# Optimization experiments

Measured on AMD Instinct MI355X. Metric: run time of the kernel, lower is better.

## Reference

```python
import jax, jax.numpy as jnp
import numpy as np

NU = 100000  # num 'user' nodes
NI = 100000  # num 'item' nodes
E = 600000   # edges per relation
IN_DIM = 128
HID = 128
OUT = 64


def setup_inputs() -> dict:
    key = jax.random.key(0)
    ks = jax.random.split(key, 14)
    return {
        "x_user": jax.random.normal(ks[0], (NU, IN_DIM), jnp.float32),
        "x_item": jax.random.normal(ks[1], (NI, IN_DIM), jnp.float32),
        "W_proj": jax.random.normal(ks[2], (IN_DIM, HID), jnp.float32) / np.sqrt(IN_DIM),
        "b_proj": jax.random.normal(ks[3], (HID,), jnp.float32) * 0.01,
        "W_out": jax.random.normal(ks[4], (HID, OUT), jnp.float32) / np.sqrt(HID),
        "b_out": jax.random.normal(ks[5], (OUT,), jnp.float32) * 0.01,
        "al1": jax.random.normal(ks[6], (1,), jnp.float32),
        "ar1": jax.random.normal(ks[7], (1,), jnp.float32),
        "al2": jax.random.normal(ks[8], (1,), jnp.float32),
        "ar2": jax.random.normal(ks[9], (1,), jnp.float32),
        "e1_src": jax.random.randint(ks[10], (E,), 0, NU, jnp.int32),  # user->user
        "e1_dst": jax.random.randint(ks[11], (E,), 0, NU, jnp.int32),
        "e2_src": jax.random.randint(ks[12], (E,), 0, NI, jnp.int32),  # item->user
        "e2_dst": jax.random.randint(ks[13], (E,), 0, NU, jnp.int32),
    }


def reference(x_user, x_item, W_proj, b_proj, W_out, b_out,
              al1, ar1, al2, ar2, e1_src, e1_dst, e2_src, e2_dst):
    # Shared projection for every node type
    h_user = x_user @ W_proj + b_proj  # [NU, HID]
    h_item = x_item @ W_proj + b_proj  # [NI, HID]

    # Relation ('user','u2u','user'): msg = h_src*al + h_dst*ar, scatter-add to dst
    msg1 = h_user[e1_src] * al1 + h_user[e1_dst] * ar1  # [E, HID]
    out_user = jax.ops.segment_sum(msg1, e1_dst, num_segments=NU)

    # Relation ('item','i2u','user')
    msg2 = h_item[e2_src] * al2 + h_user[e2_dst] * ar2  # [E, HID]
    out_user = out_user + jax.ops.segment_sum(msg2, e2_dst, num_segments=NU)

    # 'item' receives no messages -> zeros
    out_item = jnp.zeros_like(h_item)

    out_user = jax.nn.elu(out_user)
    out_item = jax.nn.elu(out_item)

    # out_layer applied only to 'user'
    out_user = out_user @ W_out + b_out  # [NU, OUT]
    return out_user, out_item
```

## Files before the change

kernel.cpp:

```cpp
#include <hip/hip_runtime.h>
#include <hip/hip_bf16.h>
#include <math.h>

#define NUSER 100000
#define NITEM 100000
#define NEDGE 600000
#define HID   128
#define OUTD  64
#define LDA   136
#define LDF   132
#define BLKR  32
#define PROJ_BLOCKS ((NUSER + NITEM) / BLKR)
#define EPB   ((2 * NEDGE) / PROJ_BLOCKS)

typedef __attribute__((ext_vector_type(8))) short  bf16x8;
typedef __attribute__((ext_vector_type(4))) float  f32x4;
typedef __attribute__((ext_vector_type(4))) unsigned short u16x4;

__device__ inline unsigned short f2bf(float f) {
    __hip_bfloat16 h = __float2bfloat16(f);
    return *reinterpret_cast<unsigned short*>(&h);
}

__device__ inline void bf2x(unsigned int u, float& lo, float& hi) {
    union { unsigned int i; float f; } a, b;
    a.i = u << 16;
    b.i = u & 0xffff0000u;
    lo = a.f; hi = b.f;
}

__global__ void prep(const float* __restrict__ W, unsigned short* __restrict__ wt,
                     int* __restrict__ deg) {
    int i = blockIdx.x * 256 + threadIdx.x;
    if (i < 2 * NUSER) deg[i] = 0;
    if (i < 128 * 128) {
        int k = i >> 7, c = i & 127;
        wt[c * 128 + k] = f2bf(W[i]);
    }
}

__device__ inline void cr_one(int i, const int* e1d, const int* e2d,
                              int* deg1, int* deg2, int* rank) {
    if (i < NEDGE)            rank[i] = atomicAdd(&deg1[e1d[i]], 1);
    else if (i < 2 * NEDGE)   rank[i] = atomicAdd(&deg2[e2d[i - NEDGE]], 1);
}

__global__ void count_rank(const int* __restrict__ e1d, const int* __restrict__ e2d,
                           int* __restrict__ deg1, int* __restrict__ deg2,
                           int* __restrict__ rank) {
    int i0 = blockIdx.x * 512 + threadIdx.x;
    cr_one(i0, e1d, e2d, deg1, deg2, rank);
    cr_one(i0 + 256, e1d, e2d, deg1, deg2, rank);
}

#define SCAN_BLOCKS 391

__global__ __launch_bounds__(256) void scanA(
    const int* __restrict__ deg1, const int* __restrict__ deg2,
    int* __restrict__ off, int* __restrict__ bsum)
{
    __shared__ int sh[256];
    int t = threadIdx.x;
    int i = blockIdx.x * 256 + t;
    int d = (i < NUSER) ? deg1[i] + deg2[i] : 0;
    sh[t] = d;
    __syncthreads();
    for (int dd = 1; dd < 256; dd <<= 1) {
        int v = (t >= dd) ? sh[t - dd] : 0;
        __syncthreads();
        sh[t] += v;
        __syncthreads();
    }
    if (i < NUSER) off[i] = (t > 0) ? sh[t - 1] : 0;
    if (t == 255) bsum[blockIdx.x] = sh[255];
}

__global__ __launch_bounds__(512) void scanB(int* __restrict__ bsum, int* __restrict__ off) {
    __shared__ int sh[512];
    int t = threadIdx.x;
    int v = (t < SCAN_BLOCKS) ? bsum[t] : 0;
    sh[t] = v;
    __syncthreads();
    for (int dd = 1; dd < 512; dd <<= 1) {
        int x = (t >= dd) ? sh[t - dd] : 0;
        __syncthreads();
        sh[t] += x;
        __syncthreads();
    }
    if (t < SCAN_BLOCKS) bsum[t] = (t > 0) ? sh[t - 1] : 0;
    if (t == 511) off[NUSER] = sh[511];
}

__global__ __launch_bounds__(256) void scanC(int* __restrict__ off, const int* __restrict__ bsum) {
    int i = blockIdx.x * 256 + threadIdx.x;
    if (i < NUSER) off[i] += bsum[blockIdx.x];
}

__global__ __launch_bounds__(256) void proj_fill(
    const float* __restrict__ xu, const float* __restrict__ xi,
    const unsigned short* __restrict__ wt, const float* __restrict__ b,
    unsigned short* __restrict__ h,
    const int* __restrict__ e1s, const int* __restrict__ e1d,
    const int* __restrict__ e2s, const int* __restrict__ e2d,
    const int* __restrict__ off, const int* __restrict__ deg1,
    const int* __restrict__ rank, int* __restrict__ adj)
{
    __shared__ unsigned short Al[BLKR * LDA];
    const int tid = threadIdx.x;
    const int r0  = blockIdx.x * BLKR;

    int fsrc = 0, fdst = -1, frank = 0, frel2 = 0;
    if (tid < EPB) {
        int i = blockIdx.x * EPB + tid;
        if (i < NEDGE) {
            fsrc = e1s[i];  fdst = e1d[i];  frank = rank[i];
        } else {
            int j = i - NEDGE;
            fsrc = NUSER + e2s[j];  fdst = e2d[j];  frank = rank[i];  frel2 = 1;
        }
    }

    float4 v[4];
    #pragma unroll
    for (int j = 0; j < 4; j++) {
        int i = tid + j * 256;
        int row = i >> 5, c4 = i & 31;
        int gr = r0 + row;
        const float* srcp = (gr < NUSER) ? xu + (size_t)gr * 128
                                         : xi + (size_t)(gr - NUSER) * 128;
        v[j] = ((const float4*)srcp)[c4];
    }
    __builtin_amdgcn_sched_barrier(0);
    #pragma unroll
    for (int j = 0; j < 4; j++) {
        int i = tid + j * 256;
        int row = i >> 5, c4 = i & 31;
        u16x4 p;
        p.x = f2bf(v[j].x); p.y = f2bf(v[j].y); p.z = f2bf(v[j].z); p.w = f2bf(v[j].w);
        *(u16x4*)&Al[row * LDA + c4 * 4] = p;
    }

    int foff = 0, fd1 = 0;
    if (fdst >= 0) {
        foff = off[fdst];
        if (frel2) fd1 = deg1[fdst];
    }
    __syncthreads();

    const int w    = tid >> 6;
    const int lane = tid & 63;
    const int lrow = lane & 15;
    const int lk   = (lane >> 4) * 8;

    bf16x8 bfrag[4][2];
    #pragma unroll
    for (int kc = 0; kc < 4; kc++) {
        const int ko = kc * 32 + lk;
        bfrag[kc][0] = *(const bf16x8*)&wt[(size_t)(w * 32 + lrow) * 128 + ko];
        bfrag[kc][1] = *(const bf16x8*)&wt[(size_t)(w * 32 + 16 + lrow) * 128 + ko];
    }

    f32x4 acc[2][2] = {};
    #pragma unroll
    for (int kc = 0; kc < 4; kc++) {
        const int ko = kc * 32 + lk;
        #pragma unroll
        for (int rt = 0; rt < 2; rt++) {
            bf16x8 aa = *(const bf16x8*)&Al[(rt * 16 + lrow) * LDA + ko];
            acc[rt][0] = __builtin_amdgcn_mfma_f32_16x16x32_bf16(aa, bfrag[kc][0], acc[rt][0], 0, 0, 0);
            acc[rt][1] = __builtin_amdgcn_mfma_f32_16x16x32_bf16(aa, bfrag[kc][1], acc[rt][1], 0, 0, 0);
        }
    }

    __syncthreads();
    const float bv0 = b[w * 32 + lrow];
    const float bv1 = b[w * 32 + 16 + lrow];
    #pragma unroll
    for (int rt = 0; rt < 2; rt++) {
        #pragma unroll
        for (int ct = 0; ct < 2; ct++) {
            int col = w * 32 + ct * 16 + lrow;
            float bv = ct ? bv1 : bv0;
            #pragma unroll
            for (int r = 0; r < 4; r++) {
                int row = rt * 16 + (lane >> 4) * 4 + r;
                Al[row * LDA + col] = f2bf(acc[rt][ct][r] + bv);
            }
        }
    }
    __syncthreads();

    #pragma unroll
    for (int j = 0; j < 2; j++) {
        int i = tid + j * 256;
        int row = i >> 4, c8 = i & 15;
        *(bf16x8*)&h[(size_t)(r0 + row) * 128 + c8 * 8] =
            *(const bf16x8*)&Al[row * LDA + c8 * 8];
    }

    if (fdst >= 0)
        adj[foff + fd1 + frank] = fsrc;
}

__global__ __launch_bounds__(256) void gather(
    const unsigned short* __restrict__ h, const int* __restrict__ adj,
    const int* __restrict__ off, const int* __restrict__ deg1,
    const int* __restrict__ deg2,
    const float* __restrict__ al1p, const float* __restrict__ ar1p,
    const float* __restrict__ al2p, const float* __restrict__ ar2p,
    unsigned int* __restrict__ accb, float* __restrict__ oitem)
{
    {
        size_t zi = (size_t)blockIdx.x * 256 + threadIdx.x;
        ((float4*)oitem)[zi] = make_float4(0.f, 0.f, 0.f, 0.f);
    }

    int wv   = (int)((blockIdx.x * 256 + threadIdx.x) >> 6);
    int lane = threadIdx.x & 63;
    if (wv >= NUSER / 2) return;
    const int nA = 2 * wv, nB = 2 * wv + 1;

    const unsigned int* h32 = (const unsigned int*)h;
    const float al1 = al1p[0], al2 = al2p[0];
    const float ar1 = ar1p[0], ar2 = ar2p[0];

    int offA = off[nA], offM = off[nA + 1], offE = off[nA + 2];
    const float scA = ar1 * (float)deg1[nA] + ar2 * (float)deg2[nA];
    const float scB = ar1 * (float)deg1[nB] + ar2 * (float)deg2[nB];

    float xA, yA, xB, yB;
    bf2x(h32[(size_t)nA * 64 + lane], xA, yA);
    bf2x(h32[(size_t)nB * 64 + lane], xB, yB);
    float sxA = scA * xA, syA = scA * yA;
    float sxB = scB * xB, syB = scB * yB;

    int eA = offA, endA = offM;
    int eB = offM, endB = offE;

    while (eA + 4 <= endA && eB + 4 <= endB) {
        int sA[4], sB[4];
        #pragma unroll
        for (int j = 0; j < 4; j++) { sA[j] = adj[eA + j]; sB[j] = adj[eB + j]; }
        unsigned int uA[4], uB[4];
        #pragma unroll
        for (int j = 0; j < 4; j++) {
            uA[j] = h32[(size_t)sA[j] * 64 + lane];
            uB[j] = h32[(size_t)sB[j] * 64 + lane];
        }
        #pragma unroll
        for (int j = 0; j < 4; j++) {
            float a = (sA[j] < NUSER) ? al1 : al2;
            float x, y; bf2x(uA[j], x, y);
            sxA = fmaf(a, x, sxA); syA = fmaf(a, y, syA);
            float b2 = (sB[j] < NUSER) ? al1 : al2;
            bf2x(uB[j], x, y);
            sxB = fmaf(b2, x, sxB); syB = fmaf(b2, y, syB);
        }
        eA += 4; eB += 4;
    }
    while (eA + 4 <= endA) {
        int s[4];
        #pragma unroll
        for (int j = 0; j < 4; j++) s[j] = adj[eA + j];
        unsigned int u[4];
        #pragma unroll
        for (int j = 0; j < 4; j++) u[j] = h32[(size_t)s[j] * 64 + lane];
        #pragma unroll
        for (int j = 0; j < 4; j++) {
            float a = (s[j] < NUSER) ? al1 : al2;
            float x, y; bf2x(u[j], x, y);
            sxA = fmaf(a, x, sxA); syA = fmaf(a, y, syA);
        }
        eA += 4;
    }
    for (; eA < endA; eA++) {
        int s0 = adj[eA];
        float a = (s0 < NUSER) ? al1 : al2;
        float x, y; bf2x(h32[(size_t)s0 * 64 + lane], x, y);
        sxA = fmaf(a, x, sxA); syA = fmaf(a, y, syA);
    }
    while (eB + 4 <= endB) {
        int s[4];
        #pragma unroll
        for (int j = 0; j < 4; j++) s[j] = adj[eB + j];
        unsigned int u[4];
        #pragma unroll
        for (int j = 0; j < 4; j++) u[j] = h32[(size_t)s[j] * 64 + lane];
        #pragma unroll
        for (int j = 0; j < 4; j++) {
            float a = (s[j] < NUSER) ? al1 : al2;
            float x, y; bf2x(u[j], x, y);
            sxB = fmaf(a, x, sxB); syB = fmaf(a, y, syB);
        }
        eB += 4;
    }
    for (; eB < endB; eB++) {
        int s0 = adj[eB];
        float a = (s0 < NUSER) ? al1 : al2;
        float x, y; bf2x(h32[(size_t)s0 * 64 + lane], x, y);
        sxB = fmaf(a, x, sxB); syB = fmaf(a, y, syB);
    }

    sxA = sxA > 0.f ? sxA : expm1f(sxA);
    syA = syA > 0.f ? syA : expm1f(syA);
    sxB = sxB > 0.f ? sxB : expm1f(sxB);
    syB = syB > 0.f ? syB : expm1f(syB);
    accb[(size_t)nA * 64 + lane] = ((unsigned int)f2bf(syA) << 16) | (unsigned int)f2bf(sxA);
    accb[(size_t)nB * 64 + lane] = ((unsigned int)f2bf(syB) << 16) | (unsigned int)f2bf(sxB);
}

__global__ __launch_bounds__(256) void finalize(
    const unsigned int* __restrict__ accb, const float* __restrict__ Wo,
    const float* __restrict__ bo, float* __restrict__ out)
{
    __shared__ float Wl[128 * 64];
    __shared__ float Al[64 * LDF];
    const int tid = threadIdx.x;
    const int n0  = blockIdx.x * 64;

    for (int i = tid; i < 128 * 64 / 4; i += 256)
        ((float4*)Wl)[i] = ((const float4*)Wo)[i];

    for (int i = tid; i < 4096; i += 256) {
        int row = i >> 6, d = i & 63;
        int gr = n0 + row;
        float lo = 0.f, hi = 0.f;
        if (gr < NUSER) bf2x(accb[(size_t)gr * 64 + d], lo, hi);
        *(float2*)&Al[row * LDF + d * 2] = make_float2(lo, hi);
    }
    __syncthreads();

    const int tr = tid >> 4;
    const int tc = tid & 15;

    float s[4][4];
    {
        float4 bv = *(const float4*)&bo[tc * 4];
        #pragma unroll
        for (int i = 0; i < 4; i++) {
            s[i][0] = bv.x; s[i][1] = bv.y; s[i][2] = bv.z; s[i][3] = bv.w;
        }
    }

    for (int k0 = 0; k0 < 128; k0 += 4) {
        float4 av[4];
        #pragma unroll
        for (int i = 0; i < 4; i++)
            av[i] = *(const float4*)&Al[(tr * 4 + i) * LDF + k0];
        #pragma unroll
        for (int kk = 0; kk < 4; kk++) {
            float4 wv = *(const float4*)&Wl[(k0 + kk) * 64 + tc * 4];
            #pragma unroll
            for (int i = 0; i < 4; i++) {
                float a = (&av[i].x)[kk];
                s[i][0] = fmaf(a, wv.x, s[i][0]);
                s[i][1] = fmaf(a, wv.y, s[i][1]);
                s[i][2] = fmaf(a, wv.z, s[i][2]);
                s[i][3] = fmaf(a, wv.w, s[i][3]);
            }
        }
    }

    #pragma unroll
    for (int i = 0; i < 4; i++) {
        int gr = n0 + tr * 4 + i;
        if (gr < NUSER) {
            float4 o = make_float4(s[i][0], s[i][1], s[i][2], s[i][3]);
            *(float4*)&out[(size_t)gr * 64 + tc * 4] = o;
        }
    }
}

extern "C" void kernel_launch(void* const* d_in, const int* in_sizes, int n_in,
                              void* d_out, int out_size, void* d_ws, size_t ws_size,
                              hipStream_t stream) {
    const float* xu  = (const float*)d_in[0];
    const float* xi  = (const float*)d_in[1];
    const float* Wp  = (const float*)d_in[2];
    const float* bp  = (const float*)d_in[3];
    const float* Wo  = (const float*)d_in[4];
    const float* bo  = (const float*)d_in[5];
    const float* al1 = (const float*)d_in[6];
    const float* ar1 = (const float*)d_in[7];
    const float* al2 = (const float*)d_in[8];
    const float* ar2 = (const float*)d_in[9];
    const int* e1s = (const int*)d_in[10];
    const int* e1d = (const int*)d_in[11];
    const int* e2s = (const int*)d_in[12];
    const int* e2d = (const int*)d_in[13];

    float* out   = (float*)d_out;
    float* oitem = out + (size_t)NUSER * OUTD;

    unsigned short* h    = (unsigned short*)d_ws;
    unsigned short* wt   = h + (size_t)(NUSER + NITEM) * HID;
    unsigned int*   accb = (unsigned int*)(wt + 128 * 128);

    int* meta = (int*)out;
    int* deg1 = meta;
    int* deg2 = meta + NUSER;
    int* off  = meta + 2 * NUSER;
    int* bsum = meta + 3 * NUSER + 64;
    int* adj  = meta + 3 * NUSER + 1024;
    int* rank = adj + 2 * NEDGE;

    prep<<<(2 * NUSER + 255) / 256, 256, 0, stream>>>(Wp, wt, deg1);

    count_rank<<<(2 * NEDGE + 511) / 512, 256, 0, stream>>>(e1d, e2d, deg1, deg2, rank);

    scanA<<<SCAN_BLOCKS, 256, 0, stream>>>(deg1, deg2, off, bsum);
    scanB<<<1, 512, 0, stream>>>(bsum, off);
    scanC<<<SCAN_BLOCKS, 256, 0, stream>>>(off, bsum);

    proj_fill<<<PROJ_BLOCKS, 256, 0, stream>>>(xu, xi, wt, bp, h,
                                               e1s, e1d, e2s, e2d,
                                               off, deg1, rank, adj);

    gather<<<(NUSER / 2 * 64) / 256, 256, 0, stream>>>(h, adj, off, deg1, deg2,
                                                       al1, ar1, al2, ar2, accb, oitem);

    finalize<<<(NUSER + 63) / 64, 256, 0, stream>>>(accb, Wo, bo, out);
}
```

Before: 229.6 us.

## Build CSR adjacency via two-level bucket binning instead of per-edge global rank atomics

```diff
diff --git a/kernel.cpp b/kernel.cpp
--- a/kernel.cpp
+++ b/kernel.cpp
@@ -11,7 +11,7 @@
 #define LDF   132
 #define BLKR  32
 #define PROJ_BLOCKS ((NUSER + NITEM) / BLKR)
-#define EPB   ((2 * NEDGE) / PROJ_BLOCKS)
+#define NB    ((NUSER + 127) / 128)
 
 typedef __attribute__((ext_vector_type(8))) short  bf16x8;
 typedef __attribute__((ext_vector_type(4))) float  f32x4;
@@ -30,27 +30,27 @@
 }
 
 __global__ void prep(const float* __restrict__ W, unsigned short* __restrict__ wt,
-                     int* __restrict__ deg) {
+                     int* __restrict__ deg, int* __restrict__ bcur) {
     int i = blockIdx.x * 256 + threadIdx.x;
     if (i < 2 * NUSER) deg[i] = 0;
+    if (i < NB) bcur[i] = 0;
     if (i < 128 * 128) {
         int k = i >> 7, c = i & 127;
         wt[c * 128 + k] = f2bf(W[i]);
     }
 }
 
-__device__ inline void cr_one(int i, const int* e1d, const int* e2d,
-                              int* deg1, int* deg2, int* rank) {
-    if (i < NEDGE)            rank[i] = atomicAdd(&deg1[e1d[i]], 1);
-    else if (i < 2 * NEDGE)   rank[i] = atomicAdd(&deg2[e2d[i - NEDGE]], 1);
-}
-
-__global__ void count_rank(const int* __restrict__ e1d, const int* __restrict__ e2d,
-                           int* __restrict__ deg1, int* __restrict__ deg2,
-                           int* __restrict__ rank) {
+__device__ inline void cd_one(int i, const int* e1d, const int* e2d,
+                              int* deg1, int* deg2) {
+    if (i < NEDGE)            atomicAdd(&deg1[e1d[i]], 1);
+    else if (i < 2 * NEDGE)   atomicAdd(&deg2[e2d[i - NEDGE]], 1);
+}
+
+__global__ void count_deg(const int* __restrict__ e1d, const int* __restrict__ e2d,
+                          int* __restrict__ deg1, int* __restrict__ deg2) {
     int i0 = blockIdx.x * 512 + threadIdx.x;
-    cr_one(i0, e1d, e2d, deg1, deg2, rank);
-    cr_one(i0 + 256, e1d, e2d, deg1, deg2, rank);
+    cd_one(i0, e1d, e2d, deg1, deg2);
+    cd_one(i0 + 256, e1d, e2d, deg1, deg2);
 }
 
 #define SCAN_BLOCKS 391
@@ -96,29 +96,61 @@
     if (i < NUSER) off[i] += bsum[blockIdx.x];
 }
 
-__global__ __launch_bounds__(256) void proj_fill(
+__global__ void bin_edges(const int* __restrict__ e1s, const int* __restrict__ e1d,
+                          const int* __restrict__ e2s, const int* __restrict__ e2d,
+                          const int* __restrict__ off, int* __restrict__ bcur,
+                          int2* __restrict__ pairs) {
+    int i = blockIdx.x * 256 + threadIdx.x;
+    if (i >= 2 * NEDGE) return;
+    int src, dst;
+    if (i < NEDGE) { src = e1s[i];                 dst = e1d[i]; }
+    else           { int j = i - NEDGE; src = NUSER + e2s[j]; dst = e2d[j]; }
+    int bkt = dst >> 7;
+    int pos = atomicAdd(&bcur[bkt], 1);
+    pairs[off[bkt << 7] + pos] = make_int2(src, dst);
+}
+
+__global__ __launch_bounds__(256) void place(
+    const int2* __restrict__ pairs, const int* __restrict__ off,
+    const int* __restrict__ deg1, int* __restrict__ adj)
+{
+    __shared__ int offL[129];
+    __shared__ int d1L[128];
+    __shared__ int cnt[256];
+    const int b  = blockIdx.x;
+    const int t  = threadIdx.x;
+    const int d0 = b << 7;
+
+    if (t < 129) {
+        int gi = d0 + t;
+        offL[t] = (gi <= NUSER) ? off[gi] : off[NUSER];
+    }
+    if (t < 128) {
+        int gi = d0 + t;
+        d1L[t] = (gi < NUSER) ? deg1[gi] : 0;
+    }
+    cnt[t] = 0;
+    __syncthreads();
+
+    const int base = offL[0];
+    const int end  = offL[128];
+    for (int e = base + t; e < end; e += 256) {
+        int2 p = pairs[e];
+        int src = p.x, dl = p.y - d0;
+        int rel = (src >= NUSER) ? 1 : 0;
+        int r = atomicAdd(&cnt[dl * 2 + rel], 1);
+        adj[offL[dl] + (rel ? d1L[dl] : 0) + r] = src;
+    }
+}
+
+__global__ __launch_bounds__(256) void proj(
     const float* __restrict__ xu, const float* __restrict__ xi,
     const unsigned short* __restrict__ wt, const float* __restrict__ b,
-    unsigned short* __restrict__ h,
-    const int* __restrict__ e1s, const int* __restrict__ e1d,
-    const int* __restrict__ e2s, const int* __restrict__ e2d,
-    const int* __restrict__ off, const int* __restrict__ deg1,
-    const int* __restrict__ rank, int* __restrict__ adj)
+    unsigned short* __restrict__ h)
 {
     __shared__ unsigned short Al[BLKR * LDA];
     const int tid = threadIdx.x;
     const int r0  = blockIdx.x * BLKR;
-
-    int fsrc = 0, fdst = -1, frank = 0, frel2 = 0;
-    if (tid < EPB) {
-        int i = blockIdx.x * EPB + tid;
-        if (i < NEDGE) {
-            fsrc = e1s[i];  fdst = e1d[i];  frank = rank[i];
-        } else {
-            int j = i - NEDGE;
-            fsrc = NUSER + e2s[j];  fdst = e2d[j];  frank = rank[i];  frel2 = 1;
-        }
-    }
 
     float4 v[4];
     #pragma unroll
@@ -138,12 +170,6 @@
         u16x4 p;
         p.x = f2bf(v[j].x); p.y = f2bf(v[j].y); p.z = f2bf(v[j].z); p.w = f2bf(v[j].w);
         *(u16x4*)&Al[row * LDA + c4 * 4] = p;
-    }
-
-    int foff = 0, fd1 = 0;
-    if (fdst >= 0) {
-        foff = off[fdst];
-        if (frel2) fd1 = deg1[fdst];
     }
     __syncthreads();
 
@@ -197,9 +223,6 @@
         *(bf16x8*)&h[(size_t)(r0 + row) * 128 + c8 * 8] =
             *(const bf16x8*)&Al[row * LDA + c8 * 8];
     }
-
-    if (fdst >= 0)
-        adj[foff + fd1 + frank] = fsrc;
 }
 
 __global__ __launch_bounds__(256) void gather(
@@ -396,25 +419,29 @@
     unsigned short* wt   = h + (size_t)(NUSER + NITEM) * HID;
     unsigned int*   accb = (unsigned int*)(wt + 128 * 128);
 
-    int* meta = (int*)out;
-    int* deg1 = meta;
-    int* deg2 = meta + NUSER;
-    int* off  = meta + 2 * NUSER;
-    int* bsum = meta + 3 * NUSER + 64;
-    int* adj  = meta + 3 * NUSER + 1024;
-    int* rank = adj + 2 * NEDGE;
-
-    prep<<<(2 * NUSER + 255) / 256, 256, 0, stream>>>(Wp, wt, deg1);
-
-    count_rank<<<(2 * NEDGE + 511) / 512, 256, 0, stream>>>(e1d, e2d, deg1, deg2, rank);
+    int* meta  = (int*)out;
+    int* deg1  = meta;
+    int* deg2  = meta + NUSER;
+    int* off   = meta + 2 * NUSER;
+    int* bsum  = meta + 3 * NUSER + 64;
+    int* adj   = meta + 3 * NUSER + 1024;
+    int2* pairs = (int2*)(adj + 2 * NEDGE);
+    int* bcur  = adj + 2 * NEDGE + 4 * NEDGE;
+
+    prep<<<(2 * NUSER + 255) / 256, 256, 0, stream>>>(Wp, wt, deg1, bcur);
+
+    count_deg<<<(2 * NEDGE + 511) / 512, 256, 0, stream>>>(e1d, e2d, deg1, deg2);
 
     scanA<<<SCAN_BLOCKS, 256, 0, stream>>>(deg1, deg2, off, bsum);
     scanB<<<1, 512, 0, stream>>>(bsum, off);
     scanC<<<SCAN_BLOCKS, 256, 0, stream>>>(off, bsum);
 
-    proj_fill<<<PROJ_BLOCKS, 256, 0, stream>>>(xu, xi, wt, bp, h,
-                                               e1s, e1d, e2s, e2d,
-                                               off, deg1, rank, adj);
+    bin_edges<<<(2 * NEDGE + 255) / 256, 256, 0, stream>>>(e1s, e1d, e2s, e2d,
+                                                           off, bcur, pairs);
+
+    place<<<NB, 256, 0, stream>>>(pairs, off, deg1, adj);
+
+    proj<<<PROJ_BLOCKS, 256, 0, stream>>>(xu, xi, wt, bp, h);
 
     gather<<<(NUSER / 2 * 64) / 256, 256, 0, stream>>>(h, adj, off, deg1, deg2,
                                                        al1, ar1, al2, ar2, accb, oitem);
```

Result: slower. 494.4 us (+115.3%).
